# Performance work log

Hardware: AMD Instinct MI355X
Metric: run time of the kernel (lower is better)

## Reference

```python
import jax, jax.numpy as jnp
import numpy as np
import math

B, H, HK, Q, K, D = 2, 64, 8, 1024, 1024, 128
HIDDEN = H * D

def setup_inputs() -> dict:
    key = jax.random.key(0)
    k1, k2, k3, k4, k5 = jax.random.split(key, 5)
    xq = jax.random.normal(k1, (B, H, Q, D), dtype=jnp.float32)
    keys = jax.random.normal(k2, (B, HK, K, D), dtype=jnp.float32)
    values = jax.random.normal(k3, (B, HK, K, D), dtype=jnp.float32)
    attn_mask = jax.random.normal(k4, (B, 1, Q, K), dtype=jnp.float32)
    wo = jax.random.normal(k5, (HIDDEN, HIDDEN), dtype=jnp.float32) * 0.02
    return {"xq": xq, "keys": keys, "values": values, "attn_mask": attn_mask, "wo": wo}

def reference(xq, keys, values, attn_mask, wo):
    b, h, q, d = xq.shape
    hk = keys.shape[1]
    g = h // hk  # GQA group size
    scale = 1.0 / math.sqrt(d)
    # expand kv heads to match query heads (group_attn_matmul semantics)
    k = jnp.repeat(keys, g, axis=1)    # [b, h, K, d]
    v = jnp.repeat(values, g, axis=1)  # [b, h, K, d]
    attn = jnp.einsum('bhqd,bhkd->bhqk', xq, k) * scale + attn_mask
    attn = jax.nn.softmax(attn, axis=-1)
    out = jnp.einsum('bhqk,bhkd->bhqd', attn, v)
    # nlp_concat_heads: [b, h, q, d] -> [b, q, h*d]
    out = out.transpose(0, 2, 1, 3).reshape(b, q, h * d)
    return out @ wo
```

## Files before the change

kernel.cpp:

```cpp
#include <hip/hip_runtime.h>
#include <hip/hip_bf16.h>
#include <stdint.h>

#define NB   2
#define NH   64
#define NHK  8
#define SQ   1024
#define SK   1024
#define DH   128
#define HID  8192
#define MROWS 2048
#define NT   128

typedef unsigned short u16;
typedef __bf16 bf16_t;
typedef bf16_t bf16x8 __attribute__((ext_vector_type(8)));
typedef float  f32x4  __attribute__((ext_vector_type(4)));
typedef u16    u16x8  __attribute__((ext_vector_type(8)));
typedef u16    u16x4  __attribute__((ext_vector_type(4)));

#define DEV __device__ __forceinline__

DEV u16 f2bf(float f) {
  uint32_t u = __builtin_bit_cast(uint32_t, f);
  u += 0x7fffu + ((u >> 16) & 1u);
  return (u16)(u >> 16);
}

DEV bf16x8 pack8(const float* v) {
  u16x8 r;
#pragma unroll
  for (int i = 0; i < 8; ++i) r[i] = f2bf(v[i]);
  return __builtin_bit_cast(bf16x8, r);
}

DEV f32x4 mfma16(bf16x8 a, bf16x8 b, f32x4 c) {
  return __builtin_amdgcn_mfma_f32_16x16x32_bf16(a, b, c, 0, 0, 0);
}

DEV void gload_lds16(const void* g, void* l) {
  __builtin_amdgcn_global_load_lds(
      (const __attribute__((address_space(1))) void*)g,
      (__attribute__((address_space(3))) void*)l, 16, 0, 0);
}

#define BAR()  asm volatile("s_barrier" ::: "memory")
#define VMC(n) asm volatile("s_waitcnt vmcnt(" #n ")" ::: "memory")

__global__ __launch_bounds__(256) void k_wo_t(const float* __restrict__ wo,
                                              u16* __restrict__ wt) {
  __shared__ u16 tile[64][72];
  const int t  = threadIdx.x;
  const int k0 = (blockIdx.x & 127) * 64;
  const int n0 = (blockIdx.x >> 7) * 64;
  const int r  = t >> 4, cg = t & 15;
#pragma unroll
  for (int p = 0; p < 4; ++p) {
    int row = r + p * 16;
    float4 v = *(const float4*)(wo + (size_t)(k0 + row) * 8192 + n0 + cg * 4);
    tile[row][cg * 4 + 0] = f2bf(v.x);
    tile[row][cg * 4 + 1] = f2bf(v.y);
    tile[row][cg * 4 + 2] = f2bf(v.z);
    tile[row][cg * 4 + 3] = f2bf(v.w);
  }
  __syncthreads();
#pragma unroll
  for (int p = 0; p < 4; ++p) {
    int row = r + p * 16;
    u16x4 ov;
    ov[0] = tile[cg * 4 + 0][row];
    ov[1] = tile[cg * 4 + 1][row];
    ov[2] = tile[cg * 4 + 2][row];
    ov[3] = tile[cg * 4 + 3][row];
    *(u16x4*)(wt + (size_t)(n0 + row) * 8192 + k0 + cg * 4) = ov;
  }
}

__global__ __launch_bounds__(256) void k_cvt_k(const float* __restrict__ keys,
                                               char* __restrict__ kf) {
  int g = blockIdx.x * 256 + threadIdx.x;
  int l    = g & 63;
  int blk  = (g >> 6) & 15;
  int t    = (g >> 10) & 15;
  int head = g >> 14;
  int ni = blk >> 2, c = blk & 3;
  int row = t * 64 + ni * 16 + (l & 15);
  int col = c * 32 + (l >> 4) * 8;
  const float* src = keys + ((size_t)head * 1024 + row) * 128 + col;
  float tb[8];
  *(float4*)tb       = *(const float4*)src;
  *(float4*)(tb + 4) = *(const float4*)(src + 4);
  u16x8 r;
#pragma unroll
  for (int i = 0; i < 8; ++i) r[i] = f2bf(tb[i]);
  *(u16x8*)(kf + (size_t)g * 16) = r;
}

__global__ __launch_bounds__(256) void k_cvt_v(const float* __restrict__ values,
                                               char* __restrict__ vf) {
  int g = blockIdx.x * 256 + threadIdx.x;
  int l    = g & 63;
  int blk  = (g >> 6) & 15;
  int t    = (g >> 10) & 15;
  int head = g >> 14;
  int ks = blk >> 3, nd = blk & 7;
  int k0 = t * 64 + ks * 32 + (l >> 4) * 8;
  int d  = nd * 16 + (l & 15);
  const float* src = values + (size_t)head * 131072 + (size_t)k0 * 128 + d;
  u16x8 r;
#pragma unroll
  for (int j = 0; j < 8; ++j) r[j] = f2bf(src[j * 128]);
  *(u16x8*)(vf + (size_t)g * 16) = r;
}

__global__ __launch_bounds__(256) void k_attn(
    const float* __restrict__ xq, const char* __restrict__ kf_g,
    const char* __restrict__ vf_g, const float* __restrict__ mask,
    u16* __restrict__ abf) {
  __shared__ u16 pl[4 * 32 * 88];

  const int b = blockIdx.z, h = blockIdx.y;
  const int q0 = blockIdx.x * 128;
  const int hk = h >> 3;
  const int tid = threadIdx.x;
  const int w = tid >> 6, l = tid & 63;
  const int lr = l & 15, lg = l >> 4;

  bf16x8 qf[2][4];
  {
    const float* qb = xq + (((size_t)(b * NH + h) * SQ) + q0 + w * 32) * DH;
#pragma unroll
    for (int mi = 0; mi < 2; ++mi)
#pragma unroll
      for (int c = 0; c < 4; ++c) {
        const float* qp = qb + (size_t)(mi * 16 + lr) * DH + c * 32 + lg * 8;
        float t[8];
        *(float4*)t       = *(const float4*)qp;
        *(float4*)(t + 4) = *(const float4*)(qp + 4);
        qf[mi][c] = pack8(t);
      }
  }

  f32x4 o[2][8];
#pragma unroll
  for (int mi = 0; mi < 2; ++mi)
#pragma unroll
    for (int nd = 0; nd < 8; ++nd) o[mi][nd] = (f32x4){0.f, 0.f, 0.f, 0.f};
  float mrun[2][4], lrun[2][4];
#pragma unroll
  for (int mi = 0; mi < 2; ++mi)
#pragma unroll
    for (int r = 0; r < 4; ++r) { mrun[mi][r] = -1e30f; lrun[mi][r] = 0.f; }

  const char* kb_base = kf_g + (size_t)(b * NHK + hk) * 262144 + l * 16;
  const char* vb_base = vf_g + (size_t)(b * NHK + hk) * 262144 + l * 16;
  const float* mk_base = mask + (size_t)b * SQ * SK;
  const float SCALE = 0.08838834764831845f;
  const float L2E   = 1.4426950408889634f;
  u16* plw = pl + w * 32 * 88;

  for (int t = 0; t < 16; ++t) {
    const int kb = t * 64;
    f32x4 s[2][4];
#pragma unroll
    for (int mi = 0; mi < 2; ++mi)
#pragma unroll
      for (int ni = 0; ni < 4; ++ni) s[mi][ni] = (f32x4){0.f, 0.f, 0.f, 0.f};
    __builtin_amdgcn_s_setprio(1);
#pragma unroll
    for (int ni = 0; ni < 4; ++ni)
#pragma unroll
      for (int c = 0; c < 4; ++c) {
        bf16x8 kf = *(const bf16x8*)(kb_base + t * 16384 + (ni * 4 + c) * 1024);
        s[0][ni] = mfma16(qf[0][c], kf, s[0][ni]);
        s[1][ni] = mfma16(qf[1][c], kf, s[1][ni]);
      }
    __builtin_amdgcn_s_setprio(0);

#pragma unroll
    for (int mi = 0; mi < 2; ++mi) {
      float x[4][4];
#pragma unroll
      for (int ni = 0; ni < 4; ++ni)
#pragma unroll
        for (int r = 0; r < 4; ++r) {
          int grow = q0 + w * 32 + mi * 16 + lg * 4 + r;
          float mv = mk_base[(size_t)grow * SK + kb + ni * 16 + lr];
          x[ni][r] = s[mi][ni][r] * SCALE + mv;
        }
      float tm[4], fac[4];
#pragma unroll
      for (int r = 0; r < 4; ++r) {
        float v = fmaxf(fmaxf(x[0][r], x[1][r]), fmaxf(x[2][r], x[3][r]));
        v = fmaxf(v, __shfl_xor(v, 1));
        v = fmaxf(v, __shfl_xor(v, 2));
        v = fmaxf(v, __shfl_xor(v, 4));
        v = fmaxf(v, __shfl_xor(v, 8));
        float mnew = fmaxf(mrun[mi][r], v);
        fac[r] = exp2f((mrun[mi][r] - mnew) * L2E);
        mrun[mi][r] = mnew;
        tm[r] = mnew;
      }
#pragma unroll
      for (int ni = 0; ni < 4; ++ni)
#pragma unroll
        for (int r = 0; r < 4; ++r) {
          float p = exp2f((x[ni][r] - tm[r]) * L2E);
          x[ni][r] = p;
          plw[(mi * 16 + lg * 4 + r) * 88 + ni * 16 + lr] = f2bf(p);
        }
#pragma unroll
      for (int r = 0; r < 4; ++r) {
        float sum = x[0][r] + x[1][r] + x[2][r] + x[3][r];
        sum += __shfl_xor(sum, 1);
        sum += __shfl_xor(sum, 2);
        sum += __shfl_xor(sum, 4);
        sum += __shfl_xor(sum, 8);
        lrun[mi][r] = lrun[mi][r] * fac[r] + sum;
      }
#pragma unroll
      for (int nd = 0; nd < 8; ++nd)
#pragma unroll
        for (int r = 0; r < 4; ++r) o[mi][nd][r] *= fac[r];
    }

    __builtin_amdgcn_s_setprio(1);
#pragma unroll
    for (int ks = 0; ks < 2; ++ks) {
      bf16x8 pf0 = *(const bf16x8*)((const char*)plw + (0 * 16 + lr) * 176 + ks * 64 + lg * 16);
      bf16x8 pf1 = *(const bf16x8*)((const char*)plw + (1 * 16 + lr) * 176 + ks * 64 + lg * 16);
#pragma unroll
      for (int nd = 0; nd < 8; ++nd) {
        bf16x8 vf = *(const bf16x8*)(vb_base + t * 16384 + (ks * 8 + nd) * 1024);
        o[0][nd] = mfma16(pf0, vf, o[0][nd]);
        o[1][nd] = mfma16(pf1, vf, o[1][nd]);
      }
    }
    __builtin_amdgcn_s_setprio(0);
  }

#pragma unroll
  for (int mi = 0; mi < 2; ++mi)
#pragma unroll
    for (int nd = 0; nd < 8; ++nd)
#pragma unroll
      for (int r = 0; r < 4; ++r) {
        int grow = q0 + w * 32 + mi * 16 + lg * 4 + r;
        size_t m = (size_t)b * SQ + grow;
        int col = h * DH + nd * 16 + lr;
        abf[m * HID + col] = f2bf(o[mi][nd][r] / lrun[mi][r]);
      }
}

__global__ __launch_bounds__(512, 2) void k_gemm(const u16* __restrict__ A,
                                                 const u16* __restrict__ Bt,
                                                 float* __restrict__ C) {
  __shared__ char L[131072];
  const int bid = blockIdx.x;
  const int logical = (bid & 7) * 32 + (bid >> 3);
  const int m0 = (logical & 7) * 256;
  const int n0 = (logical >> 3) * 256;
  const int tid = threadIdx.x;
  const int w = tid >> 6, l = tid & 63;
  const int lr = l & 15, lg = l >> 4;
  const int wm = w >> 2, wn = w & 3;

  int srow[2], scol[2];
#pragma unroll
  for (int j = 0; j < 2; ++j) {
    int ch = j * 512 + tid;
    srow[j] = ch >> 3;
    scol[j] = (ch & 7) ^ (srow[j] & 7);
  }

  const char* Ab = (const char*)A;
  const char* Bb = (const char*)Bt;

#define STAGE(gb, row0, tt, dst) do {                                          \
    int kt_ = ((tt) < NT ? (tt) : 0) * 64;                                     \
    _Pragma("unroll")                                                          \
    for (int j_ = 0; j_ < 2; ++j_)                                             \
      gload_lds16((gb) + ((size_t)((row0) + srow[j_]) * 8192 + kt_ +           \
                          scol[j_] * 8) * 2,                                   \
                  (dst) + j_ * 8192 + (w << 10));                              \
  } while (0)

#define LDA(base, hs) do {                                                     \
    _Pragma("unroll")                                                          \
    for (int mi_ = 0; mi_ < 4; ++mi_) {                                        \
      int r_ = wm * 64 + mi_ * 16 + lr;                                        \
      _Pragma("unroll")                                                        \
      for (int ks_ = 0; ks_ < 2; ++ks_)                                        \
        bA[mi_][ks_] = *(const bf16x8*)(L + (base) + (hs) * 16384 + r_ * 128 + \
                        ((ks_ * 64 + lg * 16) ^ ((r_ & 7) << 4)));             \
    }                                                                          \
  } while (0)

#define LDB(dst, base, hs) do {                                                \
    _Pragma("unroll")                                                          \
    for (int ni_ = 0; ni_ < 2; ++ni_) {                                        \
      int r_ = wn * 32 + ni_ * 16 + lr;                                        \
      _Pragma("unroll")                                                        \
      for (int ks_ = 0; ks_ < 2; ++ks_)                                        \
        dst[ni_][ks_] = *(const bf16x8*)(L + (base) + 32768 + (hs) * 16384 +   \
                        r_ * 128 + ((ks_ * 64 + lg * 16) ^ ((r_ & 7) << 4)));  \
    }                                                                          \
  } while (0)

#define MM(mh, nh, BB) do {                                                    \
    __builtin_amdgcn_s_setprio(1);                                             \
    _Pragma("unroll")                                                          \
    for (int mi_ = 0; mi_ < 4; ++mi_)                                          \
      _Pragma("unroll")                                                        \
      for (int ni_ = 0; ni_ < 2; ++ni_)                                        \
        _Pragma("unroll")                                                      \
        for (int ks_ = 0; ks_ < 2; ++ks_)                                      \
          acc[mh][nh][mi_][ni_] =                                              \
              mfma16(bA[mi_][ks_], BB[ni_][ks_], acc[mh][nh][mi_][ni_]);       \
    __builtin_amdgcn_s_setprio(0);                                             \
  } while (0)

  f32x4 acc[2][2][4][2];
#pragma unroll
  for (int a1 = 0; a1 < 2; ++a1)
#pragma unroll
    for (int a2 = 0; a2 < 2; ++a2)
#pragma unroll
      for (int a3 = 0; a3 < 4; ++a3)
#pragma unroll
        for (int a4 = 0; a4 < 2; ++a4)
          acc[a1][a2][a3][a4] = (f32x4){0.f, 0.f, 0.f, 0.f};

  bf16x8 bA[4][2], bB0[2][2], bB1[2][2];

  STAGE(Ab, m0,       0, L + 0);
  STAGE(Bb, n0,       0, L + 32768);
  STAGE(Bb, n0 + 128, 0, L + 49152);
  STAGE(Ab, m0 + 128, 0, L + 16384);
  STAGE(Ab, m0,       1, L + 65536);
  STAGE(Bb, n0,       1, L + 65536 + 32768);
  STAGE(Bb, n0 + 128, 1, L + 65536 + 49152);
  VMC(6);
  BAR();

  for (int t = 0; t < NT; ++t) {
    const int c  = (t & 1) << 16;
    const int cn = c ^ 65536;
    STAGE(Ab, m0 + 128, t + 1, L + cn + 16384);
    LDA(c, 0);
    LDB(bB0, c, 0);
    BAR();
    MM(0, 0, bB0);
    BAR();
    STAGE(Ab, m0, t + 2, L + c + 0);
    LDB(bB1, c, 1);
    BAR();
    MM(0, 1, bB1);
    BAR();
    STAGE(Bb, n0, t + 2, L + c + 32768);
    LDA(c, 1);
    BAR();
    MM(1, 1, bB1);
    BAR();
    STAGE(Bb, n0 + 128, t + 2, L + c + 49152);
    BAR();
    MM(1, 0, bB0);
    VMC(6);
    BAR();
  }
  VMC(0);

#pragma unroll
  for (int mh = 0; mh < 2; ++mh)
#pragma unroll
    for (int nh = 0; nh < 2; ++nh)
#pragma unroll
      for (int mi = 0; mi < 4; ++mi)
#pragma unroll
        for (int ni = 0; ni < 2; ++ni)
#pragma unroll
          for (int rr = 0; rr < 4; ++rr)
            C[(size_t)(m0 + mh * 128 + wm * 64 + mi * 16 + lg * 4 + rr) * 8192 +
              n0 + nh * 128 + wn * 32 + ni * 16 + lr] = acc[mh][nh][mi][ni][rr];
#undef STAGE
#undef LDA
#undef LDB
#undef MM
}

extern "C" void kernel_launch(void* const* d_in, const int* in_sizes, int n_in,
                              void* d_out, int out_size, void* d_ws, size_t ws_size,
                              hipStream_t stream) {
  const float* xq     = (const float*)d_in[0];
  const float* keys   = (const float*)d_in[1];
  const float* values = (const float*)d_in[2];
  const float* mask   = (const float*)d_in[3];
  const float* wo     = (const float*)d_in[4];
  float* out = (float*)d_out;

  char* ws = (char*)d_ws;
  u16*  Abf = (u16*)ws;
  u16*  Wt  = (u16*)(ws + 33554432ull);
  char* Kf  = ws + 33554432ull + 134217728ull;
  char* Vf  = Kf + 4194304ull;

  hipLaunchKernelGGL(k_wo_t,  dim3(16384), dim3(256), 0, stream, wo, Wt);
  hipLaunchKernelGGL(k_cvt_k, dim3(1024),  dim3(256), 0, stream, keys, Kf);
  hipLaunchKernelGGL(k_cvt_v, dim3(1024),  dim3(256), 0, stream, values, Vf);
  hipLaunchKernelGGL(k_attn,  dim3(8, 64, 2), dim3(256), 0, stream,
                     xq, Kf, Vf, mask, Abf);
  hipLaunchKernelGGL(k_gemm,  dim3(256),   dim3(512), 0, stream, Abf, Wt, out);
}
```

Baseline: 532.9 us.

## Fuse KV conversion and co-schedule wo transpose with transposed-score attention

Merges the K and V bf16 conversion kernels into one launch, and runs the wo transpose/convert blocks inside the attention launch so they fill idle CUs alongside the attention blocks. The attention computes S^T by swapping MFMA operands, so each lane owns one query row. That allows vectorized float4 mask loads, per-lane row max/sum with fewer shuffles, and a lazy rescale that only fires when the max grows by more than a threshold. P is stored to a compact XOR-swizzled LDS tile to avoid bank conflicts. The changes cut launch count, mask-load instructions and softmax overhead. The trade-offs are a heterogeneous grid and a looser running-max, which is exact in maths but could in principle overflow if masks were extreme.

```diff
diff --git a/kernel.cpp b/kernel.cpp
--- a/kernel.cpp
+++ b/kernel.cpp
@@ -47,84 +47,90 @@
 #define BAR()  asm volatile("s_barrier" ::: "memory")
 #define VMC(n) asm volatile("s_waitcnt vmcnt(" #n ")" ::: "memory")
 
-__global__ __launch_bounds__(256) void k_wo_t(const float* __restrict__ wo,
-                                              u16* __restrict__ wt) {
-  __shared__ u16 tile[64][72];
-  const int t  = threadIdx.x;
-  const int k0 = (blockIdx.x & 127) * 64;
-  const int n0 = (blockIdx.x >> 7) * 64;
-  const int r  = t >> 4, cg = t & 15;
-#pragma unroll
-  for (int p = 0; p < 4; ++p) {
-    int row = r + p * 16;
-    float4 v = *(const float4*)(wo + (size_t)(k0 + row) * 8192 + n0 + cg * 4);
-    tile[row][cg * 4 + 0] = f2bf(v.x);
-    tile[row][cg * 4 + 1] = f2bf(v.y);
-    tile[row][cg * 4 + 2] = f2bf(v.z);
-    tile[row][cg * 4 + 3] = f2bf(v.w);
-  }
-  __syncthreads();
-#pragma unroll
-  for (int p = 0; p < 4; ++p) {
-    int row = r + p * 16;
-    u16x4 ov;
-    ov[0] = tile[cg * 4 + 0][row];
-    ov[1] = tile[cg * 4 + 1][row];
-    ov[2] = tile[cg * 4 + 2][row];
-    ov[3] = tile[cg * 4 + 3][row];
-    *(u16x4*)(wt + (size_t)(n0 + row) * 8192 + k0 + cg * 4) = ov;
-  }
-}
-
-__global__ __launch_bounds__(256) void k_cvt_k(const float* __restrict__ keys,
-                                               char* __restrict__ kf) {
-  int g = blockIdx.x * 256 + threadIdx.x;
-  int l    = g & 63;
-  int blk  = (g >> 6) & 15;
-  int t    = (g >> 10) & 15;
-  int head = g >> 14;
-  int ni = blk >> 2, c = blk & 3;
-  int row = t * 64 + ni * 16 + (l & 15);
-  int col = c * 32 + (l >> 4) * 8;
-  const float* src = keys + ((size_t)head * 1024 + row) * 128 + col;
-  float tb[8];
-  *(float4*)tb       = *(const float4*)src;
-  *(float4*)(tb + 4) = *(const float4*)(src + 4);
-  u16x8 r;
-#pragma unroll
-  for (int i = 0; i < 8; ++i) r[i] = f2bf(tb[i]);
-  *(u16x8*)(kf + (size_t)g * 16) = r;
-}
-
-__global__ __launch_bounds__(256) void k_cvt_v(const float* __restrict__ values,
-                                               char* __restrict__ vf) {
-  int g = blockIdx.x * 256 + threadIdx.x;
-  int l    = g & 63;
-  int blk  = (g >> 6) & 15;
-  int t    = (g >> 10) & 15;
-  int head = g >> 14;
-  int ks = blk >> 3, nd = blk & 7;
-  int k0 = t * 64 + ks * 32 + (l >> 4) * 8;
-  int d  = nd * 16 + (l & 15);
-  const float* src = values + (size_t)head * 131072 + (size_t)k0 * 128 + d;
-  u16x8 r;
-#pragma unroll
-  for (int j = 0; j < 8; ++j) r[j] = f2bf(src[j * 128]);
-  *(u16x8*)(vf + (size_t)g * 16) = r;
-}
-
-__global__ __launch_bounds__(256) void k_attn(
+__global__ __launch_bounds__(256) void k_cvt(const float* __restrict__ keys,
+                                             const float* __restrict__ values,
+                                             char* __restrict__ kf,
+                                             char* __restrict__ vf) {
+  const int bid = blockIdx.x;
+  if (bid < 1024) {
+    int g = bid * 256 + threadIdx.x;
+    int l    = g & 63;
+    int blk  = (g >> 6) & 15;
+    int t    = (g >> 10) & 15;
+    int head = g >> 14;
+    int ni = blk >> 2, c = blk & 3;
+    int row = t * 64 + ni * 16 + (l & 15);
+    int col = c * 32 + (l >> 4) * 8;
+    const float* src = keys + ((size_t)head * 1024 + row) * 128 + col;
+    float tb[8];
+    *(float4*)tb       = *(const float4*)src;
+    *(float4*)(tb + 4) = *(const float4*)(src + 4);
+    u16x8 r;
+#pragma unroll
+    for (int i = 0; i < 8; ++i) r[i] = f2bf(tb[i]);
+    *(u16x8*)(kf + (size_t)g * 16) = r;
+  } else {
+    int g = (bid - 1024) * 256 + threadIdx.x;
+    int l    = g & 63;
+    int blk  = (g >> 6) & 15;
+    int t    = (g >> 10) & 15;
+    int head = g >> 14;
+    int ks = blk >> 3, nd = blk & 7;
+    int k0 = t * 64 + ks * 32 + (l >> 4) * 8;
+    int d  = nd * 16 + (l & 15);
+    const float* src = values + (size_t)head * 131072 + (size_t)k0 * 128 + d;
+    u16x8 r;
+#pragma unroll
+    for (int j = 0; j < 8; ++j) r[j] = f2bf(src[j * 128]);
+    *(u16x8*)(vf + (size_t)g * 16) = r;
+  }
+}
+
+__global__ __launch_bounds__(256) void k_fused(
     const float* __restrict__ xq, const char* __restrict__ kf_g,
     const char* __restrict__ vf_g, const float* __restrict__ mask,
-    u16* __restrict__ abf) {
-  __shared__ u16 pl[4 * 32 * 88];
-
-  const int b = blockIdx.z, h = blockIdx.y;
-  const int q0 = blockIdx.x * 128;
+    u16* __restrict__ abf, const float* __restrict__ wo,
+    u16* __restrict__ wt) {
+  __shared__ char smem[16384];
+  const int bid = blockIdx.x;
+  const int tid = threadIdx.x;
+
+  if (bid >= 1024) {
+    u16 (*tile)[72] = (u16 (*)[72])smem;
+    const int b2 = bid - 1024;
+    const int k0 = (b2 & 127) * 64;
+    const int n0 = (b2 >> 7) * 64;
+    const int r  = tid >> 4, cg = tid & 15;
+#pragma unroll
+    for (int p = 0; p < 4; ++p) {
+      int row = r + p * 16;
+      float4 v = *(const float4*)(wo + (size_t)(k0 + row) * 8192 + n0 + cg * 4);
+      tile[row][cg * 4 + 0] = f2bf(v.x);
+      tile[row][cg * 4 + 1] = f2bf(v.y);
+      tile[row][cg * 4 + 2] = f2bf(v.z);
+      tile[row][cg * 4 + 3] = f2bf(v.w);
+    }
+    __syncthreads();
+#pragma unroll
+    for (int p = 0; p < 4; ++p) {
+      int row = r + p * 16;
+      u16x4 ov;
+      ov[0] = tile[cg * 4 + 0][row];
+      ov[1] = tile[cg * 4 + 1][row];
+      ov[2] = tile[cg * 4 + 2][row];
+      ov[3] = tile[cg * 4 + 3][row];
+      *(u16x4*)(wt + (size_t)(n0 + row) * 8192 + k0 + cg * 4) = ov;
+    }
+    return;
+  }
+
+  const int b = bid >> 9;
+  const int h = (bid >> 3) & 63;
+  const int q0 = (bid & 7) * 128;
   const int hk = h >> 3;
-  const int tid = threadIdx.x;
   const int w = tid >> 6, l = tid & 63;
   const int lr = l & 15, lg = l >> 4;
+  char* pbyte = smem + w * 4096;
 
   bf16x8 qf[2][4];
   {
@@ -146,92 +152,97 @@
   for (int mi = 0; mi < 2; ++mi)
 #pragma unroll
     for (int nd = 0; nd < 8; ++nd) o[mi][nd] = (f32x4){0.f, 0.f, 0.f, 0.f};
-  float mrun[2][4], lrun[2][4];
-#pragma unroll
-  for (int mi = 0; mi < 2; ++mi)
-#pragma unroll
-    for (int r = 0; r < 4; ++r) { mrun[mi][r] = -1e30f; lrun[mi][r] = 0.f; }
+  float mrun[2] = {-1e30f, -1e30f}, lrun[2] = {0.f, 0.f};
 
   const char* kb_base = kf_g + (size_t)(b * NHK + hk) * 262144 + l * 16;
   const char* vb_base = vf_g + (size_t)(b * NHK + hk) * 262144 + l * 16;
   const float* mk_base = mask + (size_t)b * SQ * SK;
   const float SCALE = 0.08838834764831845f;
   const float L2E   = 1.4426950408889634f;
-  u16* plw = pl + w * 32 * 88;
+  const int rswz = (lr & 7) << 4;
 
   for (int t = 0; t < 16; ++t) {
     const int kb = t * 64;
-    f32x4 s[2][4];
+    const char* kt = kb_base + t * 16384;
+    f32x4 st[2][4];
 #pragma unroll
     for (int mi = 0; mi < 2; ++mi)
 #pragma unroll
-      for (int ni = 0; ni < 4; ++ni) s[mi][ni] = (f32x4){0.f, 0.f, 0.f, 0.f};
+      for (int ni = 0; ni < 4; ++ni) st[mi][ni] = (f32x4){0.f, 0.f, 0.f, 0.f};
     __builtin_amdgcn_s_setprio(1);
 #pragma unroll
     for (int ni = 0; ni < 4; ++ni)
 #pragma unroll
       for (int c = 0; c < 4; ++c) {
-        bf16x8 kf = *(const bf16x8*)(kb_base + t * 16384 + (ni * 4 + c) * 1024);
-        s[0][ni] = mfma16(qf[0][c], kf, s[0][ni]);
-        s[1][ni] = mfma16(qf[1][c], kf, s[1][ni]);
+        bf16x8 kf = *(const bf16x8*)(kt + (ni * 4 + c) * 1024);
+        st[0][ni] = mfma16(kf, qf[0][c], st[0][ni]);
+        st[1][ni] = mfma16(kf, qf[1][c], st[1][ni]);
       }
     __builtin_amdgcn_s_setprio(0);
 
 #pragma unroll
     for (int mi = 0; mi < 2; ++mi) {
+      const float* mrow = mk_base + (size_t)(q0 + w * 32 + mi * 16 + lr) * SK +
+                          kb + lg * 4;
       float x[4][4];
 #pragma unroll
-      for (int ni = 0; ni < 4; ++ni)
+      for (int ni = 0; ni < 4; ++ni) {
+        float4 mv = *(const float4*)(mrow + ni * 16);
+        x[ni][0] = st[mi][ni][0] * SCALE + mv.x;
+        x[ni][1] = st[mi][ni][1] * SCALE + mv.y;
+        x[ni][2] = st[mi][ni][2] * SCALE + mv.z;
+        x[ni][3] = st[mi][ni][3] * SCALE + mv.w;
+      }
+      float v = fmaxf(fmaxf(x[0][0], x[0][1]), fmaxf(x[0][2], x[0][3]));
+#pragma unroll
+      for (int ni = 1; ni < 4; ++ni)
+        v = fmaxf(v, fmaxf(fmaxf(x[ni][0], x[ni][1]),
+                           fmaxf(x[ni][2], x[ni][3])));
+      v = fmaxf(v, __shfl_xor(v, 16));
+      v = fmaxf(v, __shfl_xor(v, 32));
+      if (__any(v > mrun[mi] + 8.0f)) {
+        float mnew = fmaxf(mrun[mi], v);
+        float fac = exp2f((mrun[mi] - mnew) * L2E);
+        lrun[mi] *= fac;
+        mrun[mi] = mnew;
 #pragma unroll
         for (int r = 0; r < 4; ++r) {
-          int grow = q0 + w * 32 + mi * 16 + lg * 4 + r;
-          float mv = mk_base[(size_t)grow * SK + kb + ni * 16 + lr];
-          x[ni][r] = s[mi][ni][r] * SCALE + mv;
+          float fr = __shfl(fac, lg * 4 + r);
+#pragma unroll
+          for (int nd = 0; nd < 8; ++nd) o[mi][nd][r] *= fr;
         }
-      float tm[4], fac[4];
-#pragma unroll
-      for (int r = 0; r < 4; ++r) {
-        float v = fmaxf(fmaxf(x[0][r], x[1][r]), fmaxf(x[2][r], x[3][r]));
-        v = fmaxf(v, __shfl_xor(v, 1));
-        v = fmaxf(v, __shfl_xor(v, 2));
-        v = fmaxf(v, __shfl_xor(v, 4));
-        v = fmaxf(v, __shfl_xor(v, 8));
-        float mnew = fmaxf(mrun[mi][r], v);
-        fac[r] = exp2f((mrun[mi][r] - mnew) * L2E);
-        mrun[mi][r] = mnew;
-        tm[r] = mnew;
-      }
-#pragma unroll
-      for (int ni = 0; ni < 4; ++ni)
-#pragma unroll
-        for (int r = 0; r < 4; ++r) {
-          float p = exp2f((x[ni][r] - tm[r]) * L2E);
-          x[ni][r] = p;
-          plw[(mi * 16 + lg * 4 + r) * 88 + ni * 16 + lr] = f2bf(p);
-        }
-#pragma unroll
-      for (int r = 0; r < 4; ++r) {
-        float sum = x[0][r] + x[1][r] + x[2][r] + x[3][r];
-        sum += __shfl_xor(sum, 1);
-        sum += __shfl_xor(sum, 2);
-        sum += __shfl_xor(sum, 4);
-        sum += __shfl_xor(sum, 8);
-        lrun[mi][r] = lrun[mi][r] * fac[r] + sum;
-      }
-#pragma unroll
-      for (int nd = 0; nd < 8; ++nd)
-#pragma unroll
-        for (int r = 0; r < 4; ++r) o[mi][nd][r] *= fac[r];
+      }
+      float rs = 0.f;
+      char* prow = pbyte + (mi * 16 + lr) * 128;
+#pragma unroll
+      for (int ni = 0; ni < 4; ++ni) {
+        float p0 = exp2f((x[ni][0] - mrun[mi]) * L2E);
+        float p1 = exp2f((x[ni][1] - mrun[mi]) * L2E);
+        float p2 = exp2f((x[ni][2] - mrun[mi]) * L2E);
+        float p3 = exp2f((x[ni][3] - mrun[mi]) * L2E);
+        rs += (p0 + p1) + (p2 + p3);
+        uint32_t lo = f2bf(p0) | ((uint32_t)f2bf(p1) << 16);
+        uint32_t hi = f2bf(p2) | ((uint32_t)f2bf(p3) << 16);
+        int colb = ni * 32 + lg * 8;
+        *(uint32_t*)(prow + (colb ^ rswz)) = lo;
+        *(uint32_t*)(prow + ((colb + 4) ^ rswz)) = hi;
+      }
+      rs += __shfl_xor(rs, 16);
+      rs += __shfl_xor(rs, 32);
+      lrun[mi] += rs;
     }
 
+    const char* vt = vb_base + t * 16384;
     __builtin_amdgcn_s_setprio(1);
 #pragma unroll
     for (int ks = 0; ks < 2; ++ks) {
-      bf16x8 pf0 = *(const bf16x8*)((const char*)plw + (0 * 16 + lr) * 176 + ks * 64 + lg * 16);
-      bf16x8 pf1 = *(const bf16x8*)((const char*)plw + (1 * 16 + lr) * 176 + ks * 64 + lg * 16);
+      bf16x8 pf0 = *(const bf16x8*)(pbyte + lr * 128 +
+                                    ((ks * 64 + lg * 16) ^ rswz));
+      bf16x8 pf1 = *(const bf16x8*)(pbyte + (16 + lr) * 128 +
+                                    ((ks * 64 + lg * 16) ^ rswz));
 #pragma unroll
       for (int nd = 0; nd < 8; ++nd) {
-        bf16x8 vf = *(const bf16x8*)(vb_base + t * 16384 + (ks * 8 + nd) * 1024);
+        bf16x8 vf = *(const bf16x8*)(vt + (ks * 8 + nd) * 1024);
         o[0][nd] = mfma16(pf0, vf, o[0][nd]);
         o[1][nd] = mfma16(pf1, vf, o[1][nd]);
       }
@@ -240,7 +251,10 @@
   }
 
 #pragma unroll
-  for (int mi = 0; mi < 2; ++mi)
+  for (int mi = 0; mi < 2; ++mi) {
+    float inv[4];
+#pragma unroll
+    for (int r = 0; r < 4; ++r) inv[r] = 1.0f / __shfl(lrun[mi], lg * 4 + r);
 #pragma unroll
     for (int nd = 0; nd < 8; ++nd)
 #pragma unroll
@@ -248,8 +262,9 @@
         int grow = q0 + w * 32 + mi * 16 + lg * 4 + r;
         size_t m = (size_t)b * SQ + grow;
         int col = h * DH + nd * 16 + lr;
-        abf[m * HID + col] = f2bf(o[mi][nd][r] / lrun[mi][r]);
-      }
+        abf[m * HID + col] = f2bf(o[mi][nd][r] * inv[r]);
+      }
+  }
 }
 
 __global__ __launch_bounds__(512, 2) void k_gemm(const u16* __restrict__ A,
@@ -404,10 +419,9 @@
   char* Kf  = ws + 33554432ull + 134217728ull;
   char* Vf  = Kf + 4194304ull;
 
-  hipLaunchKernelGGL(k_wo_t,  dim3(16384), dim3(256), 0, stream, wo, Wt);
-  hipLaunchKernelGGL(k_cvt_k, dim3(1024),  dim3(256), 0, stream, keys, Kf);
-  hipLaunchKernelGGL(k_cvt_v, dim3(1024),  dim3(256), 0, stream, values, Vf);
-  hipLaunchKernelGGL(k_attn,  dim3(8, 64, 2), dim3(256), 0, stream,
-                     xq, Kf, Vf, mask, Abf);
+  hipLaunchKernelGGL(k_cvt,   dim3(2048),  dim3(256), 0, stream,
+                     keys, values, Kf, Vf);
+  hipLaunchKernelGGL(k_fused, dim3(17408), dim3(256), 0, stream,
+                     xq, Kf, Vf, mask, Abf, wo, Wt);
   hipLaunchKernelGGL(k_gemm,  dim3(256),   dim3(512), 0, stream, Abf, Wt, out);
 }
```

New measurement: 606.0 us. +13.7%, slower.
